# Kernel tuning notes

Measured on AMD Instinct MI355X. Metric: run time of the kernel, lower is better.

The kernel has to match this reference:

```python
import jax, jax.numpy as jnp
import numpy as np
from jax import lax

SMOOTH = 0.04


def setup_inputs() -> dict:
    key = jax.random.key(0)
    k1, k2 = jax.random.split(key)
    B, C, F, T = 8, 2, 257, 6000
    mag_spec = jax.random.uniform(k1, (B, C, F, T), dtype=jnp.float32)
    initial_state = jax.random.uniform(k2, (B, C, F, 1), dtype=jnp.float32)
    weights = jnp.full((1,), SMOOTH, dtype=jnp.float32)  # per_channel=False -> shape (1,)
    return {"mag_spec": mag_spec, "initial_state": initial_state, "weights": weights}


def reference(mag_spec, initial_state, weights):
    # EMA recurrence along the last (time) axis:
    #   acc_t = w * x_t + (1 - w) * acc_{t-1}
    w = jnp.clip(weights, 0.0, 1.0)  # (1,), broadcasts over [B,C,F]
    xs = jnp.moveaxis(mag_spec, -1, 0)  # [T, B, C, F]
    init = initial_state[..., 0]  # [B, C, F]

    def step(acc, x):
        acc = w * x + (1.0 - w) * acc
        return acc, acc

    _, ys = lax.scan(step, init, xs)  # ys: [T, B, C, F]
    return jnp.moveaxis(ys, 0, -1)  # [B, C, F, T]
```

## Files before the change

### kernel.cpp

```cpp
#include <hip/hip_runtime.h>


constexpr int T_LEN = 6000;
constexpr int K_PER_THREAD = 25;
constexpr int N_ACTIVE = T_LEN / K_PER_THREAD;
constexpr int BLOCK = 256;

__global__ __launch_bounds__(BLOCK) void ema_kernel(
    const float* __restrict__ x,
    const float* __restrict__ init,
    const float* __restrict__ wptr,
    float* __restrict__ out)
{
    __shared__ float tile[T_LEN];
    __shared__ float waveA[4];
    __shared__ float waveB[4];

    const int seq = blockIdx.x;
    const int tid = threadIdx.x;
    const int lane = tid & 63;
    const int wid = tid >> 6;

    const float w = fminf(fmaxf(wptr[0], 0.0f), 1.0f);
    const float d = 1.0f - w;

    const float* xs = x + (size_t)seq * T_LEN;
    float* os = out + (size_t)seq * T_LEN;

    {
        const float4* xs4 = (const float4*)xs;
        float4* tile4 = (float4*)tile;
        #pragma unroll
        for (int i = 0; i < (T_LEN / 4 + BLOCK - 1) / BLOCK; ++i) {
            int idx = tid + i * BLOCK;
            if (idx < T_LEN / 4) tile4[idx] = xs4[idx];
        }
    }
    __syncthreads();

    float A = 1.0f, B = 0.0f;
    if (tid < N_ACTIVE) {
        const int base = tid * K_PER_THREAD;
        #pragma unroll
        for (int j = 0; j < K_PER_THREAD; ++j) {
            float xv = tile[base + j];
            B = fmaf(w, xv, d * B);
            A *= d;
        }
    }

    float a = A, b = B;
    #pragma unroll
    for (int off = 1; off < 64; off <<= 1) {
        float pa = __shfl_up(a, off, 64);
        float pb = __shfl_up(b, off, 64);
        if (lane >= off) {
            b = fmaf(a, pb, b);
            a = a * pa;
        }
    }
    if (lane == 63) { waveA[wid] = a; waveB[wid] = b; }
    __syncthreads();

    float pA = 1.0f, pB = 0.0f;
    for (int i = 0; i < wid; ++i) {
        pB = fmaf(waveA[i], pB, waveB[i]);
        pA = waveA[i] * pA;
    }

    float ea = __shfl_up(a, 1, 64);
    float eb = __shfl_up(b, 1, 64);
    if (lane == 0) { ea = 1.0f; eb = 0.0f; }

    const float Aex = ea * pA;
    const float Bex = fmaf(ea, pB, eb);

    if (tid < N_ACTIVE) {
        const float s0 = init[seq];
        float acc = fmaf(Aex, s0, Bex);
        const int base = tid * K_PER_THREAD;
        #pragma unroll
        for (int j = 0; j < K_PER_THREAD; ++j) {
            acc = fmaf(w, tile[base + j], d * acc);
            tile[base + j] = acc;
        }
    }
    __syncthreads();

    {
        float4* os4 = (float4*)os;
        const float4* tile4 = (const float4*)tile;
        #pragma unroll
        for (int i = 0; i < (T_LEN / 4 + BLOCK - 1) / BLOCK; ++i) {
            int idx = tid + i * BLOCK;
            if (idx < T_LEN / 4) os4[idx] = tile4[idx];
        }
    }
}

extern "C" void kernel_launch(void* const* d_in, const int* in_sizes, int n_in,
                              void* d_out, int out_size, void* d_ws, size_t ws_size,
                              hipStream_t stream) {
    const float* mag_spec = (const float*)d_in[0];
    const float* initial_state = (const float*)d_in[1];
    const float* weights = (const float*)d_in[2];
    float* out = (float*)d_out;

    const int nseq = in_sizes[1];

    ema_kernel<<<nseq, BLOCK, 0, stream>>>(mag_spec, initial_state, weights, out);
}
```

Measured before the change: 181.0 us.

## Persistent double-buffered EMA kernel with async LDS prefetch and power-based scan

Replaces the one-block-per-sequence kernel with a persistent grid of about 768 blocks. Each block loops over several sequences and double-buffers its input: global_load_lds copies the next sequences into LDS while the current one is scanned. The scan now uses precomputed powers of (1-w), so only the B term goes through shuffles, and LDS traffic is hand-written as vectorized ds_read/ds_write_b128 with manual waitcnt. This is meant to overlap the memory-bound load and store with compute and to cut scan overhead. The cost is fragile manual vmcnt bookkeeping and a hard-coded layout of 24 elements per thread with padding.

After: 179.8 us. About the same (-0.7%).

```diff
diff --git a/kernel.cpp b/kernel.cpp
--- a/kernel.cpp
+++ b/kernel.cpp
@@ -1,100 +1,219 @@
 #include <hip/hip_runtime.h>
-
-
-constexpr int T_LEN = 6000;
-constexpr int K_PER_THREAD = 25;
-constexpr int N_ACTIVE = T_LEN / K_PER_THREAD;
-constexpr int BLOCK = 256;
-
-__global__ __launch_bounds__(BLOCK) void ema_kernel(
-    const float* __restrict__ x,
-    const float* __restrict__ init,
-    const float* __restrict__ wptr,
-    float* __restrict__ out)
+#include <stdint.h>
+
+
+constexpr int T_LEN    = 6000;
+constexpr int KPT      = 24;
+constexpr int BLOCK    = 256;
+constexpr int TILE_PAD = 6144;
+constexpr int G4       = T_LEN / 4;
+
+typedef float f32x4 __attribute__((ext_vector_type(4)));
+
+__device__ __forceinline__ uint32_t lds_off(const void* p) {
+    return (uint32_t)(uintptr_t)(const __attribute__((address_space(3))) void*)p;
+}
+
+__global__ __launch_bounds__(BLOCK) void ema_pipe(
+    const float* __restrict__ x, const float* __restrict__ init,
+    const float* __restrict__ wptr, float* __restrict__ out, int nseq)
 {
-    __shared__ float tile[T_LEN];
-    __shared__ float waveA[4];
+    __shared__ __align__(16) float tile[2][TILE_PAD];
     __shared__ float waveB[4];
 
-    const int seq = blockIdx.x;
-    const int tid = threadIdx.x;
+    const int tid  = threadIdx.x;
     const int lane = tid & 63;
-    const int wid = tid >> 6;
+    const int wid  = tid >> 6;
+    const int bid  = blockIdx.x;
+    const int G    = gridDim.x;
+    const int ns   = (nseq - bid + G - 1) / G;
+    if (ns <= 0) return;
 
     const float w = fminf(fmaxf(wptr[0], 0.0f), 1.0f);
     const float d = 1.0f - w;
 
-    const float* xs = x + (size_t)seq * T_LEN;
-    float* os = out + (size_t)seq * T_LEN;
-
-    {
-        const float4* xs4 = (const float4*)xs;
-        float4* tile4 = (float4*)tile;
+    float pw[KPT];
+    { float p = d;
+      #pragma unroll
+      for (int j = 0; j < KPT; ++j) { pw[j] = p; p *= d; } }
+    const float q = pw[KPT-1];
+    float qp[8];
+    qp[0] = q;
+    #pragma unroll
+    for (int k = 1; k < 8; ++k) qp[k] = qp[k-1] * qp[k-1];
+    const float q64 = qp[6];
+    float qlane = 1.0f;
+    #pragma unroll
+    for (int k = 0; k < 6; ++k) if ((lane >> k) & 1) qlane *= qp[k];
+    float qtid = qlane;
+    if (wid & 1) qtid *= qp[6];
+    if (wid & 2) qtid *= qp[7];
+
+    float i0=0,i1=0,i2=0,i3=0,i4=0,i5=0,i6=0,i7=0;
+    i0 = init[bid];
+    if (ns > 1) i1 = init[bid + G];
+    if (ns > 2) i2 = init[bid + 2*G];
+    if (ns > 3) i3 = init[bid + 3*G];
+    if (ns > 4) i4 = init[bid + 4*G];
+    if (ns > 5) i5 = init[bid + 5*G];
+    if (ns > 6) i6 = init[bid + 6*G];
+    if (ns > 7) i7 = init[bid + 7*G];
+
+    auto prefetch = [&](int buf, int seq) {
+        const float* src = x + (size_t)seq * T_LEN;
         #pragma unroll
-        for (int i = 0; i < (T_LEN / 4 + BLOCK - 1) / BLOCK; ++i) {
+        for (int i = 0; i < 5; ++i) {
             int idx = tid + i * BLOCK;
-            if (idx < T_LEN / 4) tile4[idx] = xs4[idx];
-        }
-    }
-    __syncthreads();
-
-    float A = 1.0f, B = 0.0f;
-    if (tid < N_ACTIVE) {
-        const int base = tid * K_PER_THREAD;
+            __builtin_amdgcn_global_load_lds(
+                (const __attribute__((address_space(1))) void*)(src + idx * 4),
+                (__attribute__((address_space(3))) void*)&tile[buf][idx * 4],
+                16, 0, 0);
+        }
+        int idx = tid + 5 * BLOCK;
+        if (idx < G4)
+            __builtin_amdgcn_global_load_lds(
+                (const __attribute__((address_space(1))) void*)(src + idx * 4),
+                (__attribute__((address_space(3))) void*)&tile[buf][idx * 4],
+                16, 0, 0);
+    };
+
+    prefetch(0, bid);
+    if (ns > 1) prefetch(1, bid + G);
+
+    for (int s = 0; s < ns; ++s) {
+        const int cur = s & 1;
+        const int seq = bid + s * G;
+
+        if (s == 0) {
+            if (ns == 1) asm volatile("s_waitcnt vmcnt(0)" ::: "memory");
+            else         asm volatile("s_waitcnt vmcnt(6)" ::: "memory");
+        } else if (s == ns - 1) {
+            asm volatile("s_waitcnt vmcnt(6)" ::: "memory");
+        } else {
+            asm volatile("s_waitcnt vmcnt(12)" ::: "memory");
+        }
+        __builtin_amdgcn_s_barrier();
+
+        float s0 = i0;
+        if (s == 1) s0 = i1;
+        if (s == 2) s0 = i2;
+        if (s == 3) s0 = i3;
+        if (s == 4) s0 = i4;
+        if (s == 5) s0 = i5;
+        if (s == 6) s0 = i6;
+        if (s == 7) s0 = i7;
+
+        f32x4 r0, r1, r2, r3, r4, r5;
+        {
+            uint32_t a = lds_off(&tile[cur][tid * KPT]);
+            asm volatile(
+                "ds_read_b128 %0, %6 offset:0\n\t"
+                "ds_read_b128 %1, %6 offset:16\n\t"
+                "ds_read_b128 %2, %6 offset:32\n\t"
+                "ds_read_b128 %3, %6 offset:48\n\t"
+                "ds_read_b128 %4, %6 offset:64\n\t"
+                "ds_read_b128 %5, %6 offset:80\n\t"
+                "s_waitcnt lgkmcnt(0)"
+                : "=&v"(r0), "=&v"(r1), "=&v"(r2), "=&v"(r3), "=&v"(r4), "=&v"(r5)
+                : "v"(a));
+        }
+        float xv[KPT];
+        xv[0]=r0.x;  xv[1]=r0.y;  xv[2]=r0.z;  xv[3]=r0.w;
+        xv[4]=r1.x;  xv[5]=r1.y;  xv[6]=r1.z;  xv[7]=r1.w;
+        xv[8]=r2.x;  xv[9]=r2.y;  xv[10]=r2.z; xv[11]=r2.w;
+        xv[12]=r3.x; xv[13]=r3.y; xv[14]=r3.z; xv[15]=r3.w;
+        xv[16]=r4.x; xv[17]=r4.y; xv[18]=r4.z; xv[19]=r4.w;
+        xv[20]=r5.x; xv[21]=r5.y; xv[22]=r5.z; xv[23]=r5.w;
+        float Bv[KPT];
+        {
+            float acc = 0.0f;
+            #pragma unroll
+            for (int j = 0; j < KPT; ++j) { acc = fmaf(w, xv[j], d * acc); Bv[j] = acc; }
+        }
+
+        float b = Bv[KPT - 1];
         #pragma unroll
-        for (int j = 0; j < K_PER_THREAD; ++j) {
-            float xv = tile[base + j];
-            B = fmaf(w, xv, d * B);
-            A *= d;
-        }
-    }
-
-    float a = A, b = B;
-    #pragma unroll
-    for (int off = 1; off < 64; off <<= 1) {
-        float pa = __shfl_up(a, off, 64);
-        float pb = __shfl_up(b, off, 64);
-        if (lane >= off) {
-            b = fmaf(a, pb, b);
-            a = a * pa;
-        }
-    }
-    if (lane == 63) { waveA[wid] = a; waveB[wid] = b; }
-    __syncthreads();
-
-    float pA = 1.0f, pB = 0.0f;
-    for (int i = 0; i < wid; ++i) {
-        pB = fmaf(waveA[i], pB, waveB[i]);
-        pA = waveA[i] * pA;
-    }
-
-    float ea = __shfl_up(a, 1, 64);
-    float eb = __shfl_up(b, 1, 64);
-    if (lane == 0) { ea = 1.0f; eb = 0.0f; }
-
-    const float Aex = ea * pA;
-    const float Bex = fmaf(ea, pB, eb);
-
-    if (tid < N_ACTIVE) {
-        const float s0 = init[seq];
-        float acc = fmaf(Aex, s0, Bex);
-        const int base = tid * K_PER_THREAD;
+        for (int k = 0; k < 6; ++k) {
+            float pb = __shfl_up(b, 1u << k, 64);
+            if (lane >= (1 << k)) b = fmaf(qp[k], pb, b);
+        }
+        if (lane == 63) {
+            uint32_t aw = lds_off(&waveB[wid]);
+            asm volatile("ds_write_b32 %0, %1" :: "v"(aw), "v"(b) : "memory");
+        }
+        asm volatile("s_waitcnt lgkmcnt(0)" ::: "memory");
+        __builtin_amdgcn_s_barrier();
+        float wb0, wb1, wb2;
+        {
+            uint32_t aw = lds_off(&waveB[0]);
+            asm volatile(
+                "ds_read_b32 %0, %3 offset:0\n\t"
+                "ds_read_b32 %1, %3 offset:4\n\t"
+                "ds_read_b32 %2, %3 offset:8\n\t"
+                "s_waitcnt lgkmcnt(0)"
+                : "=&v"(wb0), "=&v"(wb1), "=&v"(wb2)
+                : "v"(aw));
+        }
+        float pB = 0.0f;
+        if (wid > 0) pB = wb0;
+        if (wid > 1) pB = fmaf(q64, pB, wb1);
+        if (wid > 2) pB = fmaf(q64, pB, wb2);
+
+        float eb = __shfl_up(b, 1, 64);
+        if (lane == 0) eb = 0.0f;
+        const float Bex  = fmaf(qlane, pB, eb);
+        const float sin_ = fmaf(qtid, s0, Bex);
+
+        float ov[KPT];
         #pragma unroll
-        for (int j = 0; j < K_PER_THREAD; ++j) {
-            acc = fmaf(w, tile[base + j], d * acc);
-            tile[base + j] = acc;
-        }
-    }
-    __syncthreads();
-
-    {
-        float4* os4 = (float4*)os;
-        const float4* tile4 = (const float4*)tile;
-        #pragma unroll
-        for (int i = 0; i < (T_LEN / 4 + BLOCK - 1) / BLOCK; ++i) {
-            int idx = tid + i * BLOCK;
-            if (idx < T_LEN / 4) os4[idx] = tile4[idx];
-        }
+        for (int j = 0; j < KPT; ++j) ov[j] = fmaf(pw[j], sin_, Bv[j]);
+        {
+            f32x4 o0 = {ov[0],  ov[1],  ov[2],  ov[3]};
+            f32x4 o1 = {ov[4],  ov[5],  ov[6],  ov[7]};
+            f32x4 o2 = {ov[8],  ov[9],  ov[10], ov[11]};
+            f32x4 o3 = {ov[12], ov[13], ov[14], ov[15]};
+            f32x4 o4 = {ov[16], ov[17], ov[18], ov[19]};
+            f32x4 o5 = {ov[20], ov[21], ov[22], ov[23]};
+            uint32_t a = lds_off(&tile[cur][tid * KPT]);
+            asm volatile(
+                "ds_write_b128 %6, %0 offset:0\n\t"
+                "ds_write_b128 %6, %1 offset:16\n\t"
+                "ds_write_b128 %6, %2 offset:32\n\t"
+                "ds_write_b128 %6, %3 offset:48\n\t"
+                "ds_write_b128 %6, %4 offset:64\n\t"
+                "ds_write_b128 %6, %5 offset:80\n\t"
+                :
+                : "v"(o0), "v"(o1), "v"(o2), "v"(o3), "v"(o4), "v"(o5), "v"(a)
+                : "memory");
+        }
+        asm volatile("s_waitcnt lgkmcnt(0)" ::: "memory");
+        __builtin_amdgcn_s_barrier();
+
+        f32x4 v0, v1, v2, v3, v4, v5;
+        {
+            uint32_t a = lds_off(&tile[cur][0]) + (uint32_t)tid * 16u;
+            asm volatile(
+                "ds_read_b128 %0, %6 offset:0\n\t"
+                "ds_read_b128 %1, %6 offset:4096\n\t"
+                "ds_read_b128 %2, %6 offset:8192\n\t"
+                "ds_read_b128 %3, %6 offset:12288\n\t"
+                "ds_read_b128 %4, %6 offset:16384\n\t"
+                "ds_read_b128 %5, %6 offset:20480\n\t"
+                "s_waitcnt lgkmcnt(0)"
+                : "=&v"(v0), "=&v"(v1), "=&v"(v2), "=&v"(v3), "=&v"(v4), "=&v"(v5)
+                : "v"(a));
+        }
+        {
+            f32x4* os4 = (f32x4*)(out + (size_t)seq * T_LEN);
+            os4[tid]        = v0;
+            os4[tid + 256]  = v1;
+            os4[tid + 512]  = v2;
+            os4[tid + 768]  = v3;
+            os4[tid + 1024] = v4;
+            if (tid + 1280 < G4) os4[tid + 1280] = v5;
+        }
+
+        if (s + 2 < ns) prefetch(cur, bid + (s + 2) * G);
     }
 }
 
@@ -108,5 +227,9 @@
 
     const int nseq = in_sizes[1];
 
-    ema_kernel<<<nseq, BLOCK, 0, stream>>>(mag_spec, initial_state, weights, out);
+    int G = 768;
+    if ((nseq + 7) / 8 > G) G = (nseq + 7) / 8;
+    if (G > nseq) G = nseq;
+
+    ema_pipe<<<G, BLOCK, 0, stream>>>(mag_spec, initial_state, weights, out, nseq);
 }
```

## Make EMA kernel persistent with register prefetch, wave-local padded LDS and closed-form scan

Applied to the files above, without the earlier changes.

Each block now handles up to four sequences in a grid-stride loop. The next sequence is prefetched into registers while the current one is scanned and written out. Data is staged in a padded per-thread LDS layout (28 floats per 24-element chunk), so loads, chunk compute and stores stay within one wave and need only one block barrier per sequence instead of three. The scan carries only the additive term and uses precomputed powers of (1-w), so each element is touched once for the local scan and once for the fixup. The cost is higher register pressure and fewer blocks in flight.

Result: no change. 184.3 us (+1.8%).

```diff
diff --git a/kernel.cpp b/kernel.cpp
--- a/kernel.cpp
+++ b/kernel.cpp
@@ -1,99 +1,176 @@
 #include <hip/hip_runtime.h>
+#include <stdint.h>
 
 
 constexpr int T_LEN = 6000;
-constexpr int K_PER_THREAD = 25;
-constexpr int N_ACTIVE = T_LEN / K_PER_THREAD;
+constexpr int KPT   = 24;
+constexpr int NCH   = T_LEN / KPT;
 constexpr int BLOCK = 256;
+constexpr int CHW   = 28;
+constexpr int G4    = T_LEN / 4;
+
+typedef float f32x4 __attribute__((ext_vector_type(4)));
 
 __global__ __launch_bounds__(BLOCK) void ema_kernel(
-    const float* __restrict__ x,
-    const float* __restrict__ init,
-    const float* __restrict__ wptr,
-    float* __restrict__ out)
+    const float* __restrict__ x, const float* __restrict__ init,
+    const float* __restrict__ wptr, float* __restrict__ out, int nseq)
 {
-    __shared__ float tile[T_LEN];
-    __shared__ float waveA[4];
-    __shared__ float waveB[4];
+    __shared__ __align__(16) float lds[256 * CHW];
+    __shared__ float waveB[2][4];
 
-    const int seq = blockIdx.x;
-    const int tid = threadIdx.x;
+    const int tid  = threadIdx.x;
     const int lane = tid & 63;
-    const int wid = tid >> 6;
+    const int wid  = tid >> 6;
+    const int bid  = blockIdx.x;
+    const int G    = gridDim.x;
+    const int ns   = (nseq - bid + G - 1) / G;
+    if (ns <= 0) return;
 
     const float w = fminf(fmaxf(wptr[0], 0.0f), 1.0f);
     const float d = 1.0f - w;
 
-    const float* xs = x + (size_t)seq * T_LEN;
-    float* os = out + (size_t)seq * T_LEN;
+    float pw8[8];
+    { float p = d;
+      #pragma unroll
+      for (int j = 0; j < 8; ++j) { pw8[j] = p; p *= d; } }
+    const float d8 = pw8[7];
+    const float q  = d8 * d8 * d8;
+    float qp[8];
+    qp[0] = q;
+    #pragma unroll
+    for (int k = 1; k < 8; ++k) qp[k] = qp[k-1] * qp[k-1];
+    const float q64 = qp[6];
+    float qlane = 1.0f;
+    #pragma unroll
+    for (int k = 0; k < 6; ++k) if ((lane >> k) & 1) qlane *= qp[k];
+    float qtid = qlane;
+    if (wid & 1) qtid *= qp[6];
+    if (wid & 2) qtid *= qp[7];
 
+    float i0 = init[bid];
+    float i1 = (ns > 1) ? init[bid + G]     : 0.0f;
+    float i2 = (ns > 2) ? init[bid + 2 * G] : 0.0f;
+    float i3 = (ns > 3) ? init[bid + 3 * G] : 0.0f;
+
+    const int g0 = wid * 384 + lane;
+    int  woff[6];
+    bool gok[6];
+    #pragma unroll
+    for (int i = 0; i < 6; ++i) {
+        const int g = g0 + 64 * i;
+        gok[i]  = (g < G4);
+        woff[i] = CHW * (g / 6) + 4 * (g % 6);
+    }
+    const bool act   = (tid < NCH);
+    const int  cbase = CHW * tid;
+
+    f32x4 r0, r1, r2, r3, r4, r5;
     {
-        const float4* xs4 = (const float4*)xs;
-        float4* tile4 = (float4*)tile;
-        #pragma unroll
-        for (int i = 0; i < (T_LEN / 4 + BLOCK - 1) / BLOCK; ++i) {
-            int idx = tid + i * BLOCK;
-            if (idx < T_LEN / 4) tile4[idx] = xs4[idx];
-        }
-    }
-    __syncthreads();
-
-    float A = 1.0f, B = 0.0f;
-    if (tid < N_ACTIVE) {
-        const int base = tid * K_PER_THREAD;
-        #pragma unroll
-        for (int j = 0; j < K_PER_THREAD; ++j) {
-            float xv = tile[base + j];
-            B = fmaf(w, xv, d * B);
-            A *= d;
-        }
+        const f32x4* xs4 = (const f32x4*)(x + (size_t)bid * T_LEN);
+        if (gok[0]) r0 = xs4[g0];
+        if (gok[1]) r1 = xs4[g0 + 64];
+        if (gok[2]) r2 = xs4[g0 + 128];
+        if (gok[3]) r3 = xs4[g0 + 192];
+        if (gok[4]) r4 = xs4[g0 + 256];
+        if (gok[5]) r5 = xs4[g0 + 320];
     }
 
-    float a = A, b = B;
-    #pragma unroll
-    for (int off = 1; off < 64; off <<= 1) {
-        float pa = __shfl_up(a, off, 64);
-        float pb = __shfl_up(b, off, 64);
-        if (lane >= off) {
-            b = fmaf(a, pb, b);
-            a = a * pa;
+    for (int s = 0; s < ns; ++s) {
+        const int seq = bid + s * G;
+
+        if (gok[0]) *(f32x4*)&lds[woff[0]] = r0;
+        if (gok[1]) *(f32x4*)&lds[woff[1]] = r1;
+        if (gok[2]) *(f32x4*)&lds[woff[2]] = r2;
+        if (gok[3]) *(f32x4*)&lds[woff[3]] = r3;
+        if (gok[4]) *(f32x4*)&lds[woff[4]] = r4;
+        if (gok[5]) *(f32x4*)&lds[woff[5]] = r5;
+
+        float Bv[KPT];
+        float bagg = 0.0f;
+        if (act) {
+            const f32x4 c0 = *(const f32x4*)&lds[cbase];
+            const f32x4 c1 = *(const f32x4*)&lds[cbase + 4];
+            const f32x4 c2 = *(const f32x4*)&lds[cbase + 8];
+            const f32x4 c3 = *(const f32x4*)&lds[cbase + 12];
+            const f32x4 c4 = *(const f32x4*)&lds[cbase + 16];
+            const f32x4 c5 = *(const f32x4*)&lds[cbase + 20];
+            float xv[KPT];
+            xv[0]=c0.x;  xv[1]=c0.y;  xv[2]=c0.z;  xv[3]=c0.w;
+            xv[4]=c1.x;  xv[5]=c1.y;  xv[6]=c1.z;  xv[7]=c1.w;
+            xv[8]=c2.x;  xv[9]=c2.y;  xv[10]=c2.z; xv[11]=c2.w;
+            xv[12]=c3.x; xv[13]=c3.y; xv[14]=c3.z; xv[15]=c3.w;
+            xv[16]=c4.x; xv[17]=c4.y; xv[18]=c4.z; xv[19]=c4.w;
+            xv[20]=c5.x; xv[21]=c5.y; xv[22]=c5.z; xv[23]=c5.w;
+            float acc = 0.0f;
+            #pragma unroll
+            for (int j = 0; j < KPT; ++j) { acc = fmaf(d, acc, w * xv[j]); Bv[j] = acc; }
+            bagg = acc;
         }
-    }
-    if (lane == 63) { waveA[wid] = a; waveB[wid] = b; }
-    __syncthreads();
 
-    float pA = 1.0f, pB = 0.0f;
-    for (int i = 0; i < wid; ++i) {
-        pB = fmaf(waveA[i], pB, waveB[i]);
-        pA = waveA[i] * pA;
-    }
+        float b = bagg;
+        #pragma unroll
+        for (int k = 0; k < 6; ++k) {
+            const float pb = __shfl_up(b, 1u << k, 64);
+            if (lane >= (1 << k)) b = fmaf(qp[k], pb, b);
+        }
+        if (lane == 63) waveB[s & 1][wid] = b;
+        __syncthreads();
+        const float wb0 = waveB[s & 1][0];
+        const float wb1 = waveB[s & 1][1];
+        const float wb2 = waveB[s & 1][2];
+        float pB = 0.0f;
+        if (wid > 0) pB = wb0;
+        if (wid > 1) pB = fmaf(q64, pB, wb1);
+        if (wid > 2) pB = fmaf(q64, pB, wb2);
 
-    float ea = __shfl_up(a, 1, 64);
-    float eb = __shfl_up(b, 1, 64);
-    if (lane == 0) { ea = 1.0f; eb = 0.0f; }
+        float eb = __shfl_up(b, 1, 64);
+        if (lane == 0) eb = 0.0f;
+        const float Bex = fmaf(qlane, pB, eb);
+        const float s0  = (s == 0) ? i0 : (s == 1) ? i1 : (s == 2) ? i2 : i3;
+        const float sin_ = fmaf(qtid, s0, Bex);
 
-    const float Aex = ea * pA;
-    const float Bex = fmaf(ea, pB, eb);
+        if (s + 1 < ns) {
+            const f32x4* nx4 = (const f32x4*)(x + (size_t)(seq + G) * T_LEN);
+            if (gok[0]) r0 = nx4[g0];
+            if (gok[1]) r1 = nx4[g0 + 64];
+            if (gok[2]) r2 = nx4[g0 + 128];
+            if (gok[3]) r3 = nx4[g0 + 192];
+            if (gok[4]) r4 = nx4[g0 + 256];
+            if (gok[5]) r5 = nx4[g0 + 320];
+        }
 
-    if (tid < N_ACTIVE) {
-        const float s0 = init[seq];
-        float acc = fmaf(Aex, s0, Bex);
-        const int base = tid * K_PER_THREAD;
-        #pragma unroll
-        for (int j = 0; j < K_PER_THREAD; ++j) {
-            acc = fmaf(w, tile[base + j], d * acc);
-            tile[base + j] = acc;
+        if (act) {
+            const float b0 = sin_;
+            const float b1 = b0 * d8;
+            const float b2 = b1 * d8;
+            f32x4 oA = { fmaf(pw8[0],b0,Bv[0]),  fmaf(pw8[1],b0,Bv[1]),
+                         fmaf(pw8[2],b0,Bv[2]),  fmaf(pw8[3],b0,Bv[3]) };
+            f32x4 oB = { fmaf(pw8[4],b0,Bv[4]),  fmaf(pw8[5],b0,Bv[5]),
+                         fmaf(pw8[6],b0,Bv[6]),  fmaf(pw8[7],b0,Bv[7]) };
+            f32x4 oC = { fmaf(pw8[0],b1,Bv[8]),  fmaf(pw8[1],b1,Bv[9]),
+                         fmaf(pw8[2],b1,Bv[10]), fmaf(pw8[3],b1,Bv[11]) };
+            f32x4 oD = { fmaf(pw8[4],b1,Bv[12]), fmaf(pw8[5],b1,Bv[13]),
+                         fmaf(pw8[6],b1,Bv[14]), fmaf(pw8[7],b1,Bv[15]) };
+            f32x4 oE = { fmaf(pw8[0],b2,Bv[16]), fmaf(pw8[1],b2,Bv[17]),
+                         fmaf(pw8[2],b2,Bv[18]), fmaf(pw8[3],b2,Bv[19]) };
+            f32x4 oF = { fmaf(pw8[4],b2,Bv[20]), fmaf(pw8[5],b2,Bv[21]),
+                         fmaf(pw8[6],b2,Bv[22]), fmaf(pw8[7],b2,Bv[23]) };
+            *(f32x4*)&lds[cbase]      = oA;
+            *(f32x4*)&lds[cbase + 4]  = oB;
+            *(f32x4*)&lds[cbase + 8]  = oC;
+            *(f32x4*)&lds[cbase + 12] = oD;
+            *(f32x4*)&lds[cbase + 16] = oE;
+            *(f32x4*)&lds[cbase + 20] = oF;
         }
-    }
-    __syncthreads();
 
-    {
-        float4* os4 = (float4*)os;
-        const float4* tile4 = (const float4*)tile;
-        #pragma unroll
-        for (int i = 0; i < (T_LEN / 4 + BLOCK - 1) / BLOCK; ++i) {
-            int idx = tid + i * BLOCK;
-            if (idx < T_LEN / 4) os4[idx] = tile4[idx];
+        {
+            f32x4* os4 = (f32x4*)(out + (size_t)seq * T_LEN);
+            if (gok[0]) os4[g0]       = *(const f32x4*)&lds[woff[0]];
+            if (gok[1]) os4[g0 + 64]  = *(const f32x4*)&lds[woff[1]];
+            if (gok[2]) os4[g0 + 128] = *(const f32x4*)&lds[woff[2]];
+            if (gok[3]) os4[g0 + 192] = *(const f32x4*)&lds[woff[3]];
+            if (gok[4]) os4[g0 + 256] = *(const f32x4*)&lds[woff[4]];
+            if (gok[5]) os4[g0 + 320] = *(const f32x4*)&lds[woff[5]];
         }
     }
 }
@@ -108,5 +185,9 @@
 
     const int nseq = in_sizes[1];
 
-    ema_kernel<<<nseq, BLOCK, 0, stream>>>(mag_spec, initial_state, weights, out);
+    int G = (nseq + 3) / 4;
+    if (G < 1) G = 1;
+    if (G > nseq) G = nseq;
+
+    ema_kernel<<<G, BLOCK, 0, stream>>>(mag_spec, initial_state, weights, out, nseq);
 }
```

## Process one sequence per wavefront with register-pipelined chunked scan

Applied to the files above, without the earlier changes.

Each 64-lane wavefront now owns a whole sequence and handles it in 24 chunks of 256 elements, held as float4 registers with loads issued eight chunks ahead. Inside each chunk it runs a wave-level shuffle scan using precomputed decay powers and carries the running state across chunks. This drops the shared-memory tile, the block barriers and the cross-wave combine, and lets global loads overlap compute through software prefetch and sched_group_barrier hints. The cost is a serial chain of 24 shuffle scans per wave and heavy register use.

After: 191.7 us. 1.06x slower.

```diff
diff --git a/kernel.cpp b/kernel.cpp
--- a/kernel.cpp
+++ b/kernel.cpp
@@ -1,101 +1,127 @@
 #include <hip/hip_runtime.h>
+#include <stdint.h>
 
 
 constexpr int T_LEN = 6000;
-constexpr int K_PER_THREAD = 25;
-constexpr int N_ACTIVE = T_LEN / K_PER_THREAD;
 constexpr int BLOCK = 256;
 
-__global__ __launch_bounds__(BLOCK) void ema_kernel(
-    const float* __restrict__ x,
-    const float* __restrict__ init,
-    const float* __restrict__ wptr,
-    float* __restrict__ out)
+typedef float f32x4 __attribute__((ext_vector_type(4)));
+
+__global__ __launch_bounds__(BLOCK, 4) void ema_kernel(
+    const float* __restrict__ x, const float* __restrict__ init,
+    const float* __restrict__ wptr, float* __restrict__ out, int nseq)
 {
-    __shared__ float tile[T_LEN];
-    __shared__ float waveA[4];
-    __shared__ float waveB[4];
+    const int lane = threadIdx.x & 63;
+    const int wid  = threadIdx.x >> 6;
+    const int seq  = blockIdx.x * 4 + wid;
+    if (seq >= nseq) return;
 
-    const int seq = blockIdx.x;
-    const int tid = threadIdx.x;
-    const int lane = tid & 63;
-    const int wid = tid >> 6;
+    const float w  = fminf(fmaxf(wptr[0], 0.0f), 1.0f);
+    const float d  = 1.0f - w;
+    const float s0 = init[seq];
 
-    const float w = fminf(fmaxf(wptr[0], 0.0f), 1.0f);
-    const float d = 1.0f - w;
+    const f32x4* __restrict__ xs = (const f32x4*)(x   + (size_t)seq * T_LEN);
+    f32x4* __restrict__       os = (f32x4*)      (out + (size_t)seq * T_LEN);
 
-    const float* xs = x + (size_t)seq * T_LEN;
-    float* os = out + (size_t)seq * T_LEN;
+    const float pw0 = d;
+    const float pw1 = d * d;
+    const float pw2 = pw1 * d;
+    const float pw3 = pw2 * d;
+    float qp[6];
+    qp[0] = pw3;
+    #pragma unroll
+    for (int k = 1; k < 6; ++k) qp[k] = qp[k-1] * qp[k-1];
+    const float Q = qp[5] * qp[5];
+    float qlane = 1.0f;
+    #pragma unroll
+    for (int k = 0; k < 6; ++k) if ((lane >> k) & 1) qlane *= qp[k];
+
+    float c = s0;
+    float agg;
+    f32x4 o;
+
+    const int gt = (lane < 28) ? (1472 + lane) : 1499;
+
+    f32x4 r0 = xs[lane];
+    f32x4 r1 = xs[lane +  64];
+    f32x4 r2 = xs[lane + 128];
+    f32x4 r3 = xs[lane + 192];
+    f32x4 r4 = xs[lane + 256];
+    f32x4 r5 = xs[lane + 320];
+    f32x4 r6 = xs[lane + 384];
+    f32x4 r7 = xs[lane + 448];
+
+    #define GRP_BODY(xg)                                                   \
+        {                                                                  \
+            float b0 = w * (xg).x;                                         \
+            float b1 = fmaf(d, b0, w * (xg).y);                            \
+            float b2 = fmaf(d, b1, w * (xg).z);                            \
+            float b3 = fmaf(d, b2, w * (xg).w);                            \
+            float b = b3;                                                  \
+            _Pragma("unroll")                                              \
+            for (int k = 0; k < 6; ++k) {                                  \
+                float pb = __shfl_up(b, 1 << k, 64);                       \
+                if (lane >= (1 << k)) b = fmaf(qp[k], pb, b);              \
+            }                                                              \
+            float eb = __shfl_up(b, 1, 64);                                \
+            if (lane == 0) eb = 0.0f;                                      \
+            agg = __shfl(b, 63, 64);                                       \
+            const float sl = fmaf(qlane, c, eb);                           \
+            o.x = fmaf(pw0, sl, b0);                                       \
+            o.y = fmaf(pw1, sl, b1);                                       \
+            o.z = fmaf(pw2, sl, b2);                                       \
+            o.w = fmaf(pw3, sl, b3);                                       \
+        }
+
+    #define GRP_L(xg, G, GN) do {                                          \
+        GRP_BODY(xg)                                                       \
+        os[64 * (G) + lane] = o;                                           \
+        __builtin_amdgcn_sched_group_barrier(0x40, 1, 0); \
+        c = fmaf(Q, c, agg);                                               \
+        xg = xs[GN];                                                       \
+        __builtin_amdgcn_sched_group_barrier(0x20, 1, 0);  \
+    } while (0)
+
+    #define GRP_N(xg, G) do {                                              \
+        GRP_BODY(xg)                                                       \
+        os[64 * (G) + lane] = o;                                           \
+        __builtin_amdgcn_sched_group_barrier(0x40, 1, 0);                  \
+        c = fmaf(Q, c, agg);                                               \
+    } while (0)
+
+    GRP_L(r0, 0,  lane + 512);
+    GRP_L(r1, 1,  lane + 576);
+    GRP_L(r2, 2,  lane + 640);
+    GRP_L(r3, 3,  lane + 704);
+    GRP_L(r4, 4,  lane + 768);
+    GRP_L(r5, 5,  lane + 832);
+    GRP_L(r6, 6,  lane + 896);
+    GRP_L(r7, 7,  lane + 960);
+    GRP_L(r0, 8,  lane + 1024);
+    GRP_L(r1, 9,  lane + 1088);
+    GRP_L(r2, 10, lane + 1152);
+    GRP_L(r3, 11, lane + 1216);
+    GRP_L(r4, 12, lane + 1280);
+    GRP_L(r5, 13, lane + 1344);
+    GRP_L(r6, 14, lane + 1408);
+    GRP_L(r7, 15, gt);
+    GRP_N(r0, 16);
+    GRP_N(r1, 17);
+    GRP_N(r2, 18);
+    GRP_N(r3, 19);
+    GRP_N(r4, 20);
+    GRP_N(r5, 21);
+    GRP_N(r6, 22);
 
     {
-        const float4* xs4 = (const float4*)xs;
-        float4* tile4 = (float4*)tile;
-        #pragma unroll
-        for (int i = 0; i < (T_LEN / 4 + BLOCK - 1) / BLOCK; ++i) {
-            int idx = tid + i * BLOCK;
-            if (idx < T_LEN / 4) tile4[idx] = xs4[idx];
-        }
-    }
-    __syncthreads();
-
-    float A = 1.0f, B = 0.0f;
-    if (tid < N_ACTIVE) {
-        const int base = tid * K_PER_THREAD;
-        #pragma unroll
-        for (int j = 0; j < K_PER_THREAD; ++j) {
-            float xv = tile[base + j];
-            B = fmaf(w, xv, d * B);
-            A *= d;
-        }
+        GRP_BODY(r7)
+        (void)agg;
+        if (lane < 28) os[1472 + lane] = o;
     }
 
-    float a = A, b = B;
-    #pragma unroll
-    for (int off = 1; off < 64; off <<= 1) {
-        float pa = __shfl_up(a, off, 64);
-        float pb = __shfl_up(b, off, 64);
-        if (lane >= off) {
-            b = fmaf(a, pb, b);
-            a = a * pa;
-        }
-    }
-    if (lane == 63) { waveA[wid] = a; waveB[wid] = b; }
-    __syncthreads();
-
-    float pA = 1.0f, pB = 0.0f;
-    for (int i = 0; i < wid; ++i) {
-        pB = fmaf(waveA[i], pB, waveB[i]);
-        pA = waveA[i] * pA;
-    }
-
-    float ea = __shfl_up(a, 1, 64);
-    float eb = __shfl_up(b, 1, 64);
-    if (lane == 0) { ea = 1.0f; eb = 0.0f; }
-
-    const float Aex = ea * pA;
-    const float Bex = fmaf(ea, pB, eb);
-
-    if (tid < N_ACTIVE) {
-        const float s0 = init[seq];
-        float acc = fmaf(Aex, s0, Bex);
-        const int base = tid * K_PER_THREAD;
-        #pragma unroll
-        for (int j = 0; j < K_PER_THREAD; ++j) {
-            acc = fmaf(w, tile[base + j], d * acc);
-            tile[base + j] = acc;
-        }
-    }
-    __syncthreads();
-
-    {
-        float4* os4 = (float4*)os;
-        const float4* tile4 = (const float4*)tile;
-        #pragma unroll
-        for (int i = 0; i < (T_LEN / 4 + BLOCK - 1) / BLOCK; ++i) {
-            int idx = tid + i * BLOCK;
-            if (idx < T_LEN / 4) os4[idx] = tile4[idx];
-        }
-    }
+    #undef GRP_L
+    #undef GRP_N
+    #undef GRP_BODY
 }
 
 extern "C" void kernel_launch(void* const* d_in, const int* in_sizes, int n_in,
@@ -108,5 +134,6 @@
 
     const int nseq = in_sizes[1];
 
-    ema_kernel<<<nseq, BLOCK, 0, stream>>>(mag_spec, initial_state, weights, out);
+    const int G = (nseq + 3) / 4;
+    ema_kernel<<<G, BLOCK, 0, stream>>>(mag_spec, initial_state, weights, out, nseq);
 }
```
